# Kernel tuning notes

Measured on AMD Instinct MI355X. Metric: run time of the kernel, lower is better.

The kernel has to match this reference:

```python
import jax, jax.numpy as jnp
import numpy as np

N = 100000   # nodes
E = 1600000  # edges
IN = 768     # in_dim
H = 128      # hidden_dim
G = 64       # graphs per batch


def setup_inputs() -> dict:
    key = jax.random.key(0)
    ks = jax.random.split(key, 9)
    x = jax.random.normal(ks[0], (N, IN), jnp.float32)
    edge_index = jax.random.randint(ks[1], (2, E), 0, N, dtype=jnp.int64)
    batch = jnp.sort(jax.random.randint(ks[2], (N,), 0, G, dtype=jnp.int64))
    W1 = jax.random.normal(ks[3], (IN, H), jnp.float32) / np.float32(np.sqrt(IN))
    b1 = jax.random.normal(ks[4], (H,), jnp.float32) * 0.01
    W2 = jax.random.normal(ks[5], (H, H), jnp.float32) / np.float32(np.sqrt(H))
    b2 = jax.random.normal(ks[6], (H,), jnp.float32) * 0.01
    Wh = jax.random.normal(ks[7], (H, 2), jnp.float32) / np.float32(np.sqrt(H))
    bh = jax.random.normal(ks[8], (2,), jnp.float32) * 0.01
    return dict(x=x, edge_index=edge_index, batch=batch, W1=W1, b1=b1,
                W2=W2, b2=b2, Wh=Wh, bh=bh, num_graphs=G)


def gcn_conv(x, src, dst, W, b, n):
    # PyG GCNConv default: add self-loops (already in src/dst), symmetric norm.
    deg = jax.ops.segment_sum(jnp.ones_like(dst, x.dtype), dst, num_segments=n)
    dis = jnp.where(deg > 0, jax.lax.rsqrt(deg), jnp.zeros_like(deg))
    h = x @ W                                   # [n, out]
    norm = (dis[src] * dis[dst])[:, None]       # [E+n, 1]
    out = jax.ops.segment_sum(h[src] * norm, dst, num_segments=n)
    return out + b


def reference(x, edge_index, batch, W1, b1, W2, b2, Wh, bh, num_graphs):
    n = x.shape[0]
    loop = jnp.arange(n, dtype=edge_index.dtype)
    src = jnp.concatenate([edge_index[0], loop])
    dst = jnp.concatenate([edge_index[1], loop])
    h = jax.nn.relu(gcn_conv(x, src, dst, W1, b1, n))   # dropout = eval identity
    h = jax.nn.relu(gcn_conv(h, src, dst, W2, b2, n))
    summed = jax.ops.segment_sum(h, batch, num_segments=num_graphs)
    counts = jax.ops.segment_sum(jnp.ones((n, 1), h.dtype), batch, num_segments=num_graphs)
    emb = summed / jnp.maximum(counts, 1.0)             # global_mean_pool
    return emb @ Wh + bh
```

## Files before the change

kernel.cpp:

```cpp
#include <hip/hip_runtime.h>
#include <hip/hip_bf16.h>
#include <hip/hip_fp16.h>

static constexpr int N_NODES  = 100000;
static constexpr int N_EDGES  = 1600000;
static constexpr int DIM_IN   = 768;
static constexpr int DIM_H    = 128;
static constexpr int N_GRAPHS = 64;
static constexpr int NB_SCAN  = (N_NODES + 255) / 256;

typedef __attribute__((ext_vector_type(8))) _Float16 half8;
typedef __attribute__((ext_vector_type(4))) float f32x4;

__global__ void k_indeg(const int* __restrict__ edst, int* __restrict__ indeg) {
    int e = blockIdx.x * 256 + threadIdx.x;
    if (e < N_EDGES) atomicAdd(&indeg[edst[e]], 1);
}

__global__ void k_convW(const float* __restrict__ W1, const float* __restrict__ W2,
                        _Float16* __restrict__ W1t, _Float16* __restrict__ W2t) {
    int i = blockIdx.x * 256 + threadIdx.x;
    const int total1 = DIM_IN * DIM_H;
    if (i < total1) {
        int k = i >> 7, n = i & 127;
        W1t[(size_t)n * DIM_IN + k] = (_Float16)W1[i];
    } else if (i < total1 + DIM_H * DIM_H) {
        int j = i - total1;
        int k = j >> 7, n = j & 127;
        W2t[(size_t)n * DIM_H + k] = (_Float16)W2[j];
    }
}

__global__ void k_scan1(const int* __restrict__ indeg, int* __restrict__ rp,
                        int* __restrict__ bsum, float* __restrict__ dis) {
    __shared__ int s[256];
    int t = threadIdx.x;
    int i = blockIdx.x * 256 + t;
    int v = (i < N_NODES) ? indeg[i] : 0;
    s[t] = v;
    __syncthreads();
    for (int off = 1; off < 256; off <<= 1) {
        int x = (t >= off) ? s[t - off] : 0;
        __syncthreads();
        s[t] += x;
        __syncthreads();
    }
    if (i < N_NODES) {
        rp[i] = s[t] - v;
        dis[i] = rsqrtf((float)v + 1.0f);
    }
    if (t == 255) bsum[blockIdx.x] = s[255];
}

__global__ void k_scan2(int* __restrict__ bsum, const int* __restrict__ batch,
                        int* __restrict__ gstart) {
    __shared__ int s[512];
    int t = threadIdx.x;
    int v = (t < NB_SCAN) ? bsum[t] : 0;
    s[t] = v;
    __syncthreads();
    for (int off = 1; off < 512; off <<= 1) {
        int x = (t >= off) ? s[t - off] : 0;
        __syncthreads();
        s[t] += x;
        __syncthreads();
    }
    if (t < NB_SCAN) bsum[t] = s[t] - v;
    if (t <= N_GRAPHS) {
        int lo = 0, hi = N_NODES;
        while (lo < hi) {
            int mid = (lo + hi) >> 1;
            if (batch[mid] < t) lo = mid + 1; else hi = mid;
        }
        gstart[t] = lo;
    }
}

#define BKV 64
#define LDSTR 72

template<int K, bool AFP32, bool FUSE_SCATTER>
__global__ __launch_bounds__(256) void k_gemm_mfma(const void* __restrict__ Av,
                                                   const _Float16* __restrict__ Wt,
                                                   _Float16* __restrict__ C,
                                                   int nrows,
                                                   const int* __restrict__ esrc,
                                                   const int* __restrict__ edst,
                                                   const int* __restrict__ rp,
                                                   const int* __restrict__ bsum,
                                                   const float* __restrict__ dis,
                                                   int* __restrict__ cursor,
                                                   uint2* __restrict__ csrw,
                                                   int gemm_blocks) {
    __shared__ ushort As[128 * LDSTR];
    __shared__ ushort Bs[128 * LDSTR];

    if (FUSE_SCATTER && (int)blockIdx.x >= gemm_blocks) {
        int e = (blockIdx.x - gemm_blocks) * 256 + threadIdx.x;
        if (e < N_EDGES) {
            int d = edst[e];
            int sv = esrc[e];
            int pos = atomicAdd(&cursor[d], 1);
            uint2 val;
            val.x = (uint)sv;
            val.y = __float_as_uint(dis[sv]);
            csrw[rp[d] + bsum[d >> 8] + pos] = val;
        }
        return;
    }

    const int t = threadIdx.x;
    const int row0 = blockIdx.x * 128;
    const int srow = t >> 1;
    const int scol = (t & 1) * 32;
    const int l = t & 63;
    const int wv = t >> 6;
    const int wm = wv >> 1, wn = wv & 1;
    const int lr = l & 15;
    const int lk = (l >> 4) * 8;
    const bool arow_ok = (row0 + srow < nrows);

    f32x4 acc[4][4];
    const f32x4 zero = {0.f, 0.f, 0.f, 0.f};
    #pragma unroll
    for (int m = 0; m < 4; ++m)
        #pragma unroll
        for (int n = 0; n < 4; ++n) acc[m][n] = zero;

    for (int k0 = 0; k0 < K; k0 += BKV) {
        if (AFP32) {
            union { _Float16 h[32]; uint4 q[4]; } cv;
            float f[32];
            if (arow_ok) {
                const float4* Ap = (const float4*)((const float*)Av +
                    (size_t)(row0 + srow) * K + k0 + scol);
                #pragma unroll
                for (int i = 0; i < 8; ++i) *(float4*)&f[4 * i] = Ap[i];
            } else {
                #pragma unroll
                for (int i = 0; i < 32; ++i) f[i] = 0.f;
            }
            #pragma unroll
            for (int i = 0; i < 32; ++i) cv.h[i] = (_Float16)f[i];
            #pragma unroll
            for (int i = 0; i < 4; ++i)
                *(uint4*)&As[srow * LDSTR + scol + 8 * i] = cv.q[i];
        } else {
            uint4 q[4] = {{0,0,0,0},{0,0,0,0},{0,0,0,0},{0,0,0,0}};
            if (arow_ok) {
                const uint4* Ap = (const uint4*)((const _Float16*)Av +
                    (size_t)(row0 + srow) * K + k0 + scol);
                #pragma unroll
                for (int i = 0; i < 4; ++i) q[i] = Ap[i];
            }
            #pragma unroll
            for (int i = 0; i < 4; ++i)
                *(uint4*)&As[srow * LDSTR + scol + 8 * i] = q[i];
        }
        {
            const uint4* Wp = (const uint4*)(Wt + (size_t)srow * K + k0 + scol);
            #pragma unroll
            for (int i = 0; i < 4; ++i)
                *(uint4*)&Bs[srow * LDSTR + scol + 8 * i] = Wp[i];
        }
        __syncthreads();

        #pragma unroll
        for (int ks = 0; ks < BKV; ks += 32) {
            half8 a[4], b[4];
            #pragma unroll
            for (int m = 0; m < 4; ++m)
                a[m] = *(const half8*)&As[(wm * 64 + m * 16 + lr) * LDSTR + ks + lk];
            #pragma unroll
            for (int n = 0; n < 4; ++n)
                b[n] = *(const half8*)&Bs[(wn * 64 + n * 16 + lr) * LDSTR + ks + lk];
            #pragma unroll
            for (int m = 0; m < 4; ++m)
                #pragma unroll
                for (int n = 0; n < 4; ++n)
                    acc[m][n] = __builtin_amdgcn_mfma_f32_16x16x32_f16(a[m], b[n], acc[m][n], 0, 0, 0);
        }
        __syncthreads();
    }

    #pragma unroll
    for (int m = 0; m < 4; ++m) {
        #pragma unroll
        for (int n = 0; n < 4; ++n) {
            int col = wn * 64 + n * 16 + lr;
            #pragma unroll
            for (int j = 0; j < 4; ++j) {
                int row = row0 + wm * 64 + m * 16 + (l >> 4) * 4 + j;
                if (row < nrows)
                    C[(size_t)row * DIM_H + col] = (_Float16)acc[m][n][j];
            }
        }
    }
}

__device__ __forceinline__ void acc8(uint4 u, float w, float* a) {
    __half2 h0 = *(__half2*)&u.x;
    __half2 h1 = *(__half2*)&u.y;
    __half2 h2 = *(__half2*)&u.z;
    __half2 h3 = *(__half2*)&u.w;
    a[0] += __low2float(h0) * w; a[1] += __high2float(h0) * w;
    a[2] += __low2float(h1) * w; a[3] += __high2float(h1) * w;
    a[4] += __low2float(h2) * w; a[5] += __high2float(h2) * w;
    a[6] += __low2float(h3) * w; a[7] += __high2float(h3) * w;
}

__global__ __launch_bounds__(256) void k_agg(const _Float16* __restrict__ hin,
                                             const uint2* __restrict__ csrw,
                                             const int* __restrict__ rp,
                                             const int* __restrict__ bsum,
                                             const int* __restrict__ indeg,
                                             const float* __restrict__ dis,
                                             const float* __restrict__ bias,
                                             _Float16* __restrict__ hout) {
    int node = (blockIdx.x * 256 + threadIdx.x) >> 6;
    int lane = threadIdx.x & 63;
    if (node >= N_NODES) return;
    int q  = lane >> 4;
    int cl = lane & 15;
    float di = dis[node];
    int beg = rp[node] + bsum[node >> 8];
    int cnt = indeg[node];

    float a[8] = {0.f, 0.f, 0.f, 0.f, 0.f, 0.f, 0.f, 0.f};

    {
        uint s; float w;
        if (q == 0)             { s = (uint)node; w = di * di; }
        else if (q - 1 < cnt)   { uint2 p = csrw[beg + q - 1]; s = p.x; w = __uint_as_float(p.y) * di; }
        else                    { s = (uint)node; w = 0.f; }
        uint4 u = ((const uint4*)(hin + (size_t)s * DIM_H))[cl];
        acc8(u, w, a);
    }
    const uint2* cp = csrw + beg + 3;
    int m = cnt - 3;
    int i = 0;
    for (; i + 8 <= m; i += 8) {
        uint2 p0 = cp[i + q];
        uint2 p1 = cp[i + 4 + q];
        float w0 = __uint_as_float(p0.y) * di;
        float w1 = __uint_as_float(p1.y) * di;
        uint4 u0 = ((const uint4*)(hin + (size_t)p0.x * DIM_H))[cl];
        uint4 u1 = ((const uint4*)(hin + (size_t)p1.x * DIM_H))[cl];
        acc8(u0, w0, a);
        acc8(u1, w1, a);
    }
    for (; i < m; i += 4) {
        int idx = i + q;
        uint s; float w;
        if (idx < m) { uint2 p = cp[idx]; s = p.x; w = __uint_as_float(p.y) * di; }
        else         { s = (uint)node;    w = 0.f; }
        uint4 u = ((const uint4*)(hin + (size_t)s * DIM_H))[cl];
        acc8(u, w, a);
    }

    #pragma unroll
    for (int j = 0; j < 8; ++j) {
        a[j] += __shfl_xor(a[j], 16);
        a[j] += __shfl_xor(a[j], 32);
    }

    if (q == 0) {
        float4 b0 = ((const float4*)bias)[cl * 2];
        float4 b1 = ((const float4*)bias)[cl * 2 + 1];
        __half2 h0 = __floats2half2_rn(fmaxf(a[0] + b0.x, 0.f), fmaxf(a[1] + b0.y, 0.f));
        __half2 h1 = __floats2half2_rn(fmaxf(a[2] + b0.z, 0.f), fmaxf(a[3] + b0.w, 0.f));
        __half2 h2 = __floats2half2_rn(fmaxf(a[4] + b1.x, 0.f), fmaxf(a[5] + b1.y, 0.f));
        __half2 h3 = __floats2half2_rn(fmaxf(a[6] + b1.z, 0.f), fmaxf(a[7] + b1.w, 0.f));
        uint4 o;
        o.x = *(uint*)&h0; o.y = *(uint*)&h1; o.z = *(uint*)&h2; o.w = *(uint*)&h3;
        ((uint4*)(hout + (size_t)node * DIM_H))[cl] = o;
    }
}

#define PSPLIT 8
__global__ __launch_bounds__(256) void k_pool(const _Float16* __restrict__ h,
                                              const int* __restrict__ gstart,
                                              float* __restrict__ pooled2) {
    int g  = blockIdx.x >> 3;
    int sp = blockIdx.x & 7;
    int r0 = gstart[g], r1 = gstart[g + 1];
    int count = r1 - r0;
    int chunk = (count + PSPLIT - 1) / PSPLIT;
    int aS = r0 + sp * chunk;
    int bE = min(aS + chunk, r1);
    int c  = threadIdx.x & 63;
    int rr = threadIdx.x >> 6;
    float s0a = 0.f, s1a = 0.f, s0b = 0.f, s1b = 0.f;
    int r = aS + rr;
    for (; r + 4 < bE; r += 8) {
        uint ua = ((const uint*)(h + (size_t)r * DIM_H))[c];
        uint ub = ((const uint*)(h + (size_t)(r + 4) * DIM_H))[c];
        __half2 ha = *(__half2*)&ua;
        __half2 hb = *(__half2*)&ub;
        s0a += __low2float(ha); s1a += __high2float(ha);
        s0b += __low2float(hb); s1b += __high2float(hb);
    }
    if (r < bE) {
        uint ua = ((const uint*)(h + (size_t)r * DIM_H))[c];
        __half2 ha = *(__half2*)&ua;
        s0a += __low2float(ha); s1a += __high2float(ha);
    }
    float s0 = s0a + s0b, s1 = s1a + s1b;
    __shared__ float sm0[4][64], sm1[4][64];
    sm0[rr][c] = s0; sm1[rr][c] = s1;
    __syncthreads();
    if (rr == 0) {
        float v0 = sm0[0][c] + sm0[1][c] + sm0[2][c] + sm0[3][c];
        float v1 = sm1[0][c] + sm1[1][c] + sm1[2][c] + sm1[3][c];
        float* dst = pooled2 + (size_t)(g * PSPLIT + sp) * DIM_H;
        dst[2 * c]     = v0;
        dst[2 * c + 1] = v1;
    }
}

__global__ __launch_bounds__(128) void k_head(const float* __restrict__ pooled2,
                                              const int* __restrict__ gstart,
                                              const float* __restrict__ Wh,
                                              const float* __restrict__ bh,
                                              float* __restrict__ out) {
    int g = blockIdx.x;
    int c = threadIdx.x;
    float s = 0.f;
    #pragma unroll
    for (int sp = 0; sp < PSPLIT; ++sp)
        s += pooled2[(size_t)(g * PSPLIT + sp) * DIM_H + c];
    float cntg = (float)(gstart[g + 1] - gstart[g]);
    float e = s / fmaxf(cntg, 1.0f);
    __shared__ float s0[128], s1[128];
    s0[c] = e * Wh[c * 2 + 0];
    s1[c] = e * Wh[c * 2 + 1];
    __syncthreads();
    for (int off = 64; off > 0; off >>= 1) {
        if (c < off) { s0[c] += s0[c + off]; s1[c] += s1[c + off]; }
        __syncthreads();
    }
    if (c == 0) {
        out[g * 2 + 0] = s0[0] + bh[0];
        out[g * 2 + 1] = s1[0] + bh[1];
    }
}

extern "C" void kernel_launch(void* const* d_in, const int* in_sizes, int n_in,
                              void* d_out, int out_size, void* d_ws, size_t ws_size,
                              hipStream_t stream) {
    const float* x    = (const float*)d_in[0];
    const int*   esrc = (const int*)d_in[1];
    const int*   edst = esrc + N_EDGES;
    const int*   batch= (const int*)d_in[2];
    const float* W1   = (const float*)d_in[3];
    const float* b1   = (const float*)d_in[4];
    const float* W2   = (const float*)d_in[5];
    const float* b2   = (const float*)d_in[6];
    const float* Wh   = (const float*)d_in[7];
    const float* bh   = (const float*)d_in[8];
    float* out = (float*)d_out;

    char* ws = (char*)d_ws;
    size_t off = 0;
    auto alloc = [&](size_t bytes) {
        void* p = ws + off;
        off += (bytes + 255) & ~(size_t)255;
        return p;
    };
    _Float16* bufZ   = (_Float16*)alloc((size_t)N_NODES * DIM_H * 2);
    _Float16* bufH   = (_Float16*)alloc((size_t)N_NODES * DIM_H * 2);
    float*    dis    = (float*)alloc((size_t)N_NODES * 4);
    int*      deg2   = (int*)  alloc((size_t)2 * N_NODES * 4);
    int*      indeg  = deg2;
    int*      cursor = deg2 + N_NODES;
    int*      rp     = (int*)  alloc((size_t)N_NODES * 4);
    uint2*    csrw   = (uint2*)alloc((size_t)N_EDGES * 8);
    int*      bsum   = (int*)  alloc(512 * 4);
    float*    pooled2= (float*)alloc((size_t)N_GRAPHS * PSPLIT * DIM_H * 4);
    int*      gstart = (int*)  alloc((N_GRAPHS + 1) * 4);
    _Float16* W1t    = (_Float16*)alloc((size_t)DIM_IN * DIM_H * 2);
    _Float16* W2t    = (_Float16*)alloc((size_t)DIM_H * DIM_H * 2);

    hipMemsetAsync(deg2, 0, (size_t)2 * N_NODES * 4, stream);

    int convblocks = (DIM_IN * DIM_H + DIM_H * DIM_H + 255) / 256;
    k_convW  <<<convblocks, 256, 0, stream>>>(W1, W2, W1t, W2t);

    k_indeg  <<<(N_EDGES + 255) / 256, 256, 0, stream>>>(edst, indeg);
    k_scan1  <<<NB_SCAN, 256, 0, stream>>>(indeg, rp, bsum, dis);
    k_scan2  <<<1, 512, 0, stream>>>(bsum, batch, gstart);

    int gblocks = (N_NODES + 127) / 128;
    int scblocks = (N_EDGES + 255) / 256;
    k_gemm_mfma<DIM_IN, true, true><<<gblocks + scblocks, 256, 0, stream>>>(
        x, W1t, bufZ, N_NODES, esrc, edst, rp, bsum, dis, cursor, csrw, gblocks);
    k_agg<<<(N_NODES + 3) / 4, 256, 0, stream>>>(bufZ, csrw, rp, bsum, indeg, dis, b1, bufH);
    k_gemm_mfma<DIM_H, false, false><<<gblocks, 256, 0, stream>>>(
        bufH, W2t, bufZ, N_NODES, nullptr, nullptr, nullptr, nullptr, nullptr, nullptr, nullptr, gblocks);
    k_agg<<<(N_NODES + 3) / 4, 256, 0, stream>>>(bufZ, csrw, rp, bsum, indeg, dis, b2, bufH);

    k_pool<<<N_GRAPHS * PSPLIT, 256, 0, stream>>>(bufH, gstart, pooled2);
    k_head<<<N_GRAPHS, 128, 0, stream>>>(pooled2, gstart, Wh, bh, out);
}
```

Before: 417.1 us.

## Load GEMM A fragments directly from global memory, dropping A shared-memory staging

```diff
diff --git a/kernel.cpp b/kernel.cpp
--- a/kernel.cpp
+++ b/kernel.cpp
@@ -77,7 +77,7 @@
 }
 
 #define BKV 64
-#define LDSTR 72
+#define WLDSTR 72
 
 template<int K, bool AFP32, bool FUSE_SCATTER>
 __global__ __launch_bounds__(256) void k_gemm_mfma(const void* __restrict__ Av,
@@ -92,8 +92,7 @@
                                                    int* __restrict__ cursor,
                                                    uint2* __restrict__ csrw,
                                                    int gemm_blocks) {
-    __shared__ ushort As[128 * LDSTR];
-    __shared__ ushort Bs[128 * LDSTR];
+    __shared__ ushort Bs[128 * WLDSTR];
 
     if (FUSE_SCATTER && (int)blockIdx.x >= gemm_blocks) {
         int e = (blockIdx.x - gemm_blocks) * 256 + threadIdx.x;
@@ -117,8 +116,7 @@
     const int wv = t >> 6;
     const int wm = wv >> 1, wn = wv & 1;
     const int lr = l & 15;
-    const int lk = (l >> 4) * 8;
-    const bool arow_ok = (row0 + srow < nrows);
+    const int lk8 = (l >> 4) * 8;
 
     f32x4 acc[4][4];
     const f32x4 zero = {0.f, 0.f, 0.f, 0.f};
@@ -127,58 +125,51 @@
         #pragma unroll
         for (int n = 0; n < 4; ++n) acc[m][n] = zero;
 
+    int arow[4];
+    #pragma unroll
+    for (int m = 0; m < 4; ++m)
+        arow[m] = min(row0 + wm * 64 + m * 16 + lr, nrows - 1);
+
     for (int k0 = 0; k0 < K; k0 += BKV) {
-        if (AFP32) {
-            union { _Float16 h[32]; uint4 q[4]; } cv;
-            float f[32];
-            if (arow_ok) {
-                const float4* Ap = (const float4*)((const float*)Av +
-                    (size_t)(row0 + srow) * K + k0 + scol);
-                #pragma unroll
-                for (int i = 0; i < 8; ++i) *(float4*)&f[4 * i] = Ap[i];
-            } else {
-                #pragma unroll
-                for (int i = 0; i < 32; ++i) f[i] = 0.f;
+        {
+            const uint4* Wp = (const uint4*)(Wt + (size_t)srow * K + k0 + scol);
+            uint4 w0 = Wp[0], w1 = Wp[1], w2 = Wp[2], w3 = Wp[3];
+            *(uint4*)&Bs[srow * WLDSTR + scol + 0]  = w0;
+            *(uint4*)&Bs[srow * WLDSTR + scol + 8]  = w1;
+            *(uint4*)&Bs[srow * WLDSTR + scol + 16] = w2;
+            *(uint4*)&Bs[srow * WLDSTR + scol + 24] = w3;
+        }
+        __syncthreads();
+
+        #pragma unroll
+        for (int ks2 = 0; ks2 < 2; ++ks2) {
+            half8 afr[4], bfr[4];
+            #pragma unroll
+            for (int m = 0; m < 4; ++m) {
+                if (AFP32) {
+                    const float* ap = (const float*)Av +
+                        (size_t)arow[m] * K + k0 + ks2 * 32 + lk8;
+                    float4 x0 = *(const float4*)ap;
+                    float4 x1 = *(const float4*)(ap + 4);
+                    half8 r;
+                    r[0] = (_Float16)x0.x; r[1] = (_Float16)x0.y;
+                    r[2] = (_Float16)x0.z; r[3] = (_Float16)x0.w;
+                    r[4] = (_Float16)x1.x; r[5] = (_Float16)x1.y;
+                    r[6] = (_Float16)x1.z; r[7] = (_Float16)x1.w;
+                    afr[m] = r;
+                } else {
+                    afr[m] = *(const half8*)((const _Float16*)Av +
+                        (size_t)arow[m] * K + k0 + ks2 * 32 + lk8);
+                }
             }
             #pragma unroll
-            for (int i = 0; i < 32; ++i) cv.h[i] = (_Float16)f[i];
-            #pragma unroll
-            for (int i = 0; i < 4; ++i)
-                *(uint4*)&As[srow * LDSTR + scol + 8 * i] = cv.q[i];
-        } else {
-            uint4 q[4] = {{0,0,0,0},{0,0,0,0},{0,0,0,0},{0,0,0,0}};
-            if (arow_ok) {
-                const uint4* Ap = (const uint4*)((const _Float16*)Av +
-                    (size_t)(row0 + srow) * K + k0 + scol);
-                #pragma unroll
-                for (int i = 0; i < 4; ++i) q[i] = Ap[i];
-            }
-            #pragma unroll
-            for (int i = 0; i < 4; ++i)
-                *(uint4*)&As[srow * LDSTR + scol + 8 * i] = q[i];
-        }
-        {
-            const uint4* Wp = (const uint4*)(Wt + (size_t)srow * K + k0 + scol);
-            #pragma unroll
-            for (int i = 0; i < 4; ++i)
-                *(uint4*)&Bs[srow * LDSTR + scol + 8 * i] = Wp[i];
-        }
-        __syncthreads();
-
-        #pragma unroll
-        for (int ks = 0; ks < BKV; ks += 32) {
-            half8 a[4], b[4];
-            #pragma unroll
-            for (int m = 0; m < 4; ++m)
-                a[m] = *(const half8*)&As[(wm * 64 + m * 16 + lr) * LDSTR + ks + lk];
-            #pragma unroll
             for (int n = 0; n < 4; ++n)
-                b[n] = *(const half8*)&Bs[(wn * 64 + n * 16 + lr) * LDSTR + ks + lk];
+                bfr[n] = *(const half8*)&Bs[(wn * 64 + n * 16 + lr) * WLDSTR + ks2 * 32 + lk8];
             #pragma unroll
             for (int m = 0; m < 4; ++m)
                 #pragma unroll
                 for (int n = 0; n < 4; ++n)
-                    acc[m][n] = __builtin_amdgcn_mfma_f32_16x16x32_f16(a[m], b[n], acc[m][n], 0, 0, 0);
+                    acc[m][n] = __builtin_amdgcn_mfma_f32_16x16x32_f16(afr[m], bfr[n], acc[m][n], 0, 0, 0);
         }
         __syncthreads();
     }
```

Result: slower. 429.7 us (+3.0%).
